# Kernel tuning notes

Measured on AMD Instinct MI355X. Metric: run time of the kernel, lower is better.

The kernel has to match this reference:

```python
import jax, jax.numpy as jnp
import numpy as np

BETA = 0.99
TOL = 1e-4
MAX_ITER = 1000
EPS = 1e-3
B, N, HF, HV, KV = 65536, 32, 25, 128, 8


def fhat(x, fp):
    W1, b1, W2, b2, W3, b3 = fp
    h = jax.nn.softplus(x @ W1 + b1)
    h = jax.nn.softplus(h @ W2 + b2)
    return h @ W3 + b3  # (B,1,N)


def V(z, vp):
    # Lyapunov function: V(z) = ||g(z)-g(0)||^2 + eps*||z||^2 ; V(0)=0, V>0 elsewhere.
    W1, b1, W2, b2, W3, b3 = vp
    def mlp(u):
        h = jax.nn.softplus(u @ W1 + b1)
        h = jax.nn.softplus(h @ W2 + b2)
        return h @ W3 + b3
    h = mlp(z)
    h0 = mlp(jnp.zeros((1, 1, z.shape[-1]), z.dtype))
    return (jnp.sum((h - h0) ** 2, axis=-1, keepdims=True)
            + EPS * jnp.sum(z * z, axis=-1, keepdims=True))  # (B,1,1)


def newton_F(fhatx, target, gamma, vp):
    # F = gamma - (V(fhatx*gamma)-target)/dV_dgamma  (newton_iter.forward)
    Vg, dV = jax.jvp(lambda g: V(fhatx * g, vp), (gamma,), (jnp.ones_like(gamma),))
    return gamma - (Vg - target) / dV


def solve_gamma(fhatx, target, vp):
    # Vectorized masked Newton + bisection (rootfind_train.forward).
    gamma = jnp.ones((fhatx.shape[0], 1, 1), fhatx.dtype)
    e1 = jnp.zeros_like(gamma)
    e2 = jnp.ones_like(gamma)
    active = (V(fhatx, vp) - target) > 0.0  # samples needing rootfind

    def cond(s):
        return jnp.logical_and(jnp.any(s[3]), s[4] < MAX_ITER)

    def body(s):
        gamma, e1, e2, m, it = s
        # Newton step on active, unconverged samples
        newt = newton_F(fhatx, target, gamma, vp)
        gamma = jnp.where(m, newt, gamma)
        # bisection backup where Newton left [e1,e2] (or produced non-finite)
        m_bisec = m & ((gamma < e1) | (gamma > e2) | ~jnp.isfinite(gamma))
        a = 0.5 * (e1 + e2)
        s_a = jnp.sign(V(fhatx * a, vp) - target)
        s_1 = jnp.sign(V(fhatx * e1, vp) - target)
        s_2 = jnp.sign(V(fhatx * e2, vp) - target)
        e2 = jnp.where(m_bisec & (s_a * s_1 < 0), a, e2)
        e1 = jnp.where(m_bisec & (s_a * s_2 < 0), a, e1)
        gamma = jnp.where(m_bisec, a, gamma)
        m = active & (jnp.abs(V(fhatx * gamma, vp) - target) > TOL)
        return (gamma, e1, e2, m, it + 1)

    gamma = jax.lax.while_loop(cond, body, (gamma, e1, e2, active, jnp.int32(0)))[0]
    return gamma


@jax.jit
def _forward(x, fp, vp):
    fhatx = fhat(x, fp)
    target = BETA * V(x, vp)
    viol = V(fhatx, vp) > target  # these go through rootfind; rest pass through fhat
    gamma = solve_gamma(fhatx, target, vp)
    return jnp.where(viol, fhatx * gamma, fhatx)


def setup_inputs() -> dict:
    key = jax.random.key(0)
    ks = jax.random.split(key, 13)
    def w(k, shape, fan):
        return jax.random.normal(k, shape, jnp.float32) / np.float32(np.sqrt(fan))
    return {
        'x': jax.random.normal(ks[0], (B, 1, N), jnp.float32),
        'f_W1': w(ks[1], (N, HF), N), 'f_b1': jnp.zeros((HF,), jnp.float32),
        'f_W2': w(ks[2], (HF, HF), HF), 'f_b2': jnp.zeros((HF,), jnp.float32),
        'f_W3': w(ks[3], (HF, N), HF), 'f_b3': jnp.zeros((N,), jnp.float32),
        'v_W1': w(ks[4], (N, HV), N), 'v_b1': jnp.zeros((HV,), jnp.float32),
        'v_W2': w(ks[5], (HV, HV), HV), 'v_b2': jnp.zeros((HV,), jnp.float32),
        'v_W3': w(ks[6], (HV, KV), HV), 'v_b3': jnp.zeros((KV,), jnp.float32),
    }


def reference(x, f_W1, f_b1, f_W2, f_b2, f_W3, f_b3,
              v_W1, v_b1, v_W2, v_b2, v_W3, v_b3):
    fp = (f_W1, f_b1, f_W2, f_b2, f_W3, f_b3)
    vp = (v_W1, v_b1, v_W2, v_b2, v_W3, v_b3)
    return _forward(x, fp, vp)
```

## Files before the change

### kernel.cpp

```cpp
#include <hip/hip_runtime.h>
#include <math.h>

#define BETA_C   0.99f
#define TOL_C    1e-4f
#define ACC_C    2e-3f
#define BRK_C    2e-3f
#define FORCE_C  6
#define MAXIT_C  1000
#define EPS_C    1e-3f
#define BN       65536
#define NN       32
#define HFD      25
#define HVD      128
#define KVD      8
#define G        16
#define GPB      16
#define SGPB     16
#define SBLK     256
#define NQBLK    768


typedef __attribute__((ext_vector_type(8))) short bf16x8;
typedef __attribute__((ext_vector_type(8))) unsigned short u16x8;
typedef __attribute__((ext_vector_type(4))) float f32x4;

__device__ __forceinline__ void wsync() {
    __builtin_amdgcn_wave_barrier();
    __threadfence_block();
    __builtin_amdgcn_wave_barrier();
}

__device__ __forceinline__ float sp_(float x) {
    return fmaxf(x, 0.f) + log1pf(expf(-fabsf(x)));
}
__device__ __forceinline__ float spf_(float x) {
    return fmaxf(x, 0.f) + __logf(1.f + __expf(-fabsf(x)));
}
__device__ __forceinline__ float sgn_(float d) {
    return (d > 0.f) ? 1.f : ((d < 0.f) ? -1.f : 0.f);
}
__device__ __forceinline__ unsigned short f2bf(float f) {
    unsigned int u = __float_as_uint(f);
    u += 0x7FFFu + ((u >> 16) & 1u);
    return (unsigned short)(u >> 16);
}
__device__ __forceinline__ float bf2f(unsigned short u) {
    return __uint_as_float(((unsigned int)u) << 16);
}

__device__ __forceinline__ void aw_st(unsigned short* aw, int row, int col, float v) {
    const int b = (row * 64 + col * 2) ^ ((row & 3) << 4);
    *(unsigned short*)((char*)aw + b) = f2bf(v);
}
__device__ __forceinline__ bf16x8 aw_ld(const unsigned short* aw, int row, int k) {
    const int b = (row * 64 + k * 2) ^ ((row & 3) << 4);
    return *(const bf16x8*)((const char*)aw + b);
}
__device__ __forceinline__ void hw_st(unsigned short* hw, int row, int col, float v) {
    const int b = (row * 256 + col * 2) ^ ((row & 7) << 4);
    *(unsigned short*)((char*)hw + b) = f2bf(v);
}
__device__ __forceinline__ bf16x8 hw_ld(const unsigned short* hw, int row, int k) {
    const int b = (row * 256 + k * 2) ^ ((row & 7) << 4);
    return *(const bf16x8*)((const char*)hw + b);
}

__device__ __forceinline__ void veval2_sec(
    const int gl, const float (&uA)[8], const float (&uB)[8],
    const float gA, const float gB,
    float2* h1q, const float n2A, const float n2B,
    const float (&b1v)[8], const float (&b2v)[8], const float (&d0c)[8],
    const unsigned short* w2L, const unsigned short* __restrict__ w3s,
    float& VA, float& VB)
{
    const int k0 = gl * 8;
#pragma unroll
    for (int j = 0; j < 8; ++j) {
        const float preA = fmaf(gA, uA[j], b1v[j]);
        const float preB = fmaf(gB, uB[j], b1v[j]);
        h1q[(j << 4) | gl] = make_float2(spf_(preA), spf_(preB));
    }
    wsync();
    float aA[8], aB[8];
#pragma unroll
    for (int j = 0; j < 8; ++j) { aA[j] = 0.f; aB[j] = 0.f; }
#pragma unroll 4
    for (int k = 0; k < HVD; ++k) {
        const float2 q = h1q[((k & 7) << 4) | (k >> 3)];
        const u16x8 wv = *(const u16x8*)(w2L + k * HVD + k0);
#pragma unroll
        for (int j = 0; j < 8; ++j) {
            const float w = bf2f(wv[j]);
            aA[j] = fmaf(q.x, w, aA[j]);
            aB[j] = fmaf(q.y, w, aB[j]);
        }
    }
    wsync();
    float oA[KVD], oB[KVD];
#pragma unroll
    for (int c = 0; c < KVD; ++c) { oA[c] = 0.f; oB[c] = 0.f; }
#pragma unroll
    for (int j = 0; j < 8; ++j) {
        const float h2A = spf_(aA[j] + b2v[j]);
        const float h2B = spf_(aB[j] + b2v[j]);
        const u16x8 w3v = *(const u16x8*)(w3s + (k0 + j) * KVD);
#pragma unroll
        for (int c = 0; c < 8; ++c) {
            const float w3 = bf2f(w3v[c]);
            oA[c] = fmaf(h2A, w3, oA[c]);
            oB[c] = fmaf(h2B, w3, oB[c]);
        }
    }
#pragma unroll
    for (int m = 1; m < G; m <<= 1) {
#pragma unroll
        for (int c = 0; c < KVD; ++c) {
            oA[c] += __shfl_xor(oA[c], m);
            oB[c] += __shfl_xor(oB[c], m);
        }
    }
    float vvA = 0.f, vvB = 0.f;
#pragma unroll
    for (int c = 0; c < KVD; ++c) {
        const float eA = oA[c] + d0c[c];
        const float eB = oB[c] + d0c[c];
        vvA = fmaf(eA, eA, vvA);
        vvB = fmaf(eB, eB, vvB);
    }
    VA = vvA + EPS_C * gA * gA * n2A;
    VB = vvB + EPS_C * gB * gB * n2B;
}

__global__ __launch_bounds__(256, 2) void k_wprep(
    const float* __restrict__ vW1, const float* __restrict__ vW2,
    const float* __restrict__ vW3,
    const float* __restrict__ vb1, const float* __restrict__ vb2,
    const float* __restrict__ vb3,
    unsigned short* __restrict__ w1b, unsigned short* __restrict__ w2b,
    unsigned short* __restrict__ w3b,
    unsigned short* __restrict__ w2s, unsigned short* __restrict__ w3s,
    float* __restrict__ h0g)
{
    if (blockIdx.x == 32) {
        __shared__ float h1s[HVD];
        __shared__ float h2p[2][HVD];
        __shared__ float h2s[HVD];
        __shared__ float o3p[16][KVD + 1];
        const int t = threadIdx.x;
        if (t < HVD) h1s[t] = sp_(vb1[t]);
        __syncthreads();
        {
            const int j = t & 127, half = t >> 7;
            float a = half ? 0.f : vb2[j];
            const int kb = half * 64;
            for (int k = 0; k < 64; ++k)
                a = fmaf(h1s[kb + k], vW2[(kb + k) * HVD + j], a);
            h2p[half][j] = a;
        }
        __syncthreads();
        if (t < HVD) h2s[t] = sp_(h2p[0][t] + h2p[1][t]);
        __syncthreads();
        if (t < 128) {
            const int c = t & 7, ch = t >> 3;
            float a = 0.f;
            for (int k = ch * 8; k < ch * 8 + 8; ++k)
                a = fmaf(h2s[k], vW3[k * KVD + c], a);
            o3p[ch][c] = a;
        }
        __syncthreads();
        if (t < KVD) {
            float acc = vb3[t];
            for (int ch = 0; ch < 16; ++ch) acc += o3p[ch][t];
            h0g[t] = acc;
        }
        return;
    }
    const int t = blockIdx.x * 256 + threadIdx.x;
    const int nth = 32 * 256;
    for (int i = t; i < HVD * NN; i += nth) {
        const int col = i >> 5, k = i & 31;
        w1b[i] = f2bf(vW1[k * HVD + col]);
    }
    for (int i = t; i < HVD * HVD; i += nth) {
        const int col = i >> 7, k = i & 127;
        w2b[i] = f2bf(vW2[k * HVD + col]);
    }
    for (int i = t; i < 16 * HVD; i += nth) {
        const int c = i >> 7, k = i & 127;
        w3b[i] = (c < KVD) ? f2bf(vW3[k * KVD + c]) : (unsigned short)0;
    }
    for (int i = t; i < HVD * HVD; i += nth)
        w2s[i] = f2bf(vW2[i]);
    for (int i = t; i < HVD * KVD; i += nth)
        w3s[i] = f2bf(vW3[i]);
}

__global__ __launch_bounds__(256, 2) void k_setup(
    const float* __restrict__ x_g,
    const float* __restrict__ fW1, const float* __restrict__ fb1,
    const float* __restrict__ fW2, const float* __restrict__ fb2,
    const float* __restrict__ fW3, const float* __restrict__ fb3,
    const float* __restrict__ vb1, const float* __restrict__ vb2,
    const float* __restrict__ vb3,
    const unsigned short* __restrict__ w1b,
    const unsigned short* __restrict__ w2b,
    const unsigned short* __restrict__ w3b,
    const float* __restrict__ h0g,
    float* __restrict__ out,
    int* __restrict__ cnt, int* __restrict__ list, float* __restrict__ tgt,
    float* __restrict__ vfb)
{
    __shared__ float2 xs[GPB][NN + 1];
    __shared__ float2 fh1[GPB][HFD + 1];
    __shared__ float2 fh2[GPB][HFD + 1];
    __shared__ __align__(16) unsigned short abf[4][16 * 32];
    __shared__ __align__(16) unsigned short hbf[4][16 * HVD];
    __shared__ int wcnt[4];
    __shared__ int bbase;

    const int tid = threadIdx.x;
    const int gi = tid >> 4;
    const int gl = tid & (G - 1);
    const int w  = tid >> 6;
    const int l  = tid & 63;
    const int q  = l >> 4;
    const int cc = l & 15;
    const int sb = (blockIdx.x * GPB + gi) * 2;
    const int s0 = sb, s1 = sb + 1;
    unsigned short* aw = abf[w];
    unsigned short* hw = hbf[w];

    const float xa0 = x_g[(size_t)s0 * NN + gl];
    const float xa1 = x_g[(size_t)s0 * NN + gl + 16];
    const float xb0 = x_g[(size_t)s1 * NN + gl];
    const float xb1 = x_g[(size_t)s1 * NN + gl + 16];
    xs[gi][gl]      = make_float2(xa0, xb0);
    xs[gi][gl + 16] = make_float2(xa1, xb1);
    const int r0 = 4 * q;
    aw_st(aw, r0,     gl,      xa0); aw_st(aw, r0,     gl + 16, xa1);
    aw_st(aw, r0 + 2, gl,      xb0); aw_st(aw, r0 + 2, gl + 16, xb1);
    wsync();

    float fA0, fA1, fB0, fB1;
    {
        const int uu0 = gl;
        const int uu1 = gl + G;
        const bool u1v = (uu1 < HFD);
        const int uu1c = u1v ? uu1 : (HFD - 1);
        float a0 = fb1[uu0], a1 = a0;
        float c0 = fb1[uu1c], c1 = c0;
#pragma unroll
        for (int i = 0; i < NN; ++i) {
            const float2 xv2 = xs[gi][i];
            const float w0 = fW1[i * HFD + uu0];
            const float w1 = fW1[i * HFD + uu1c];
            a0 = fmaf(xv2.x, w0, a0);
            a1 = fmaf(xv2.y, w0, a1);
            c0 = fmaf(xv2.x, w1, c0);
            c1 = fmaf(xv2.y, w1, c1);
        }
        fh1[gi][uu0] = make_float2(spf_(a0), spf_(a1));
        if (u1v) fh1[gi][uu1] = make_float2(spf_(c0), spf_(c1));
        wsync();
        a0 = fb2[uu0]; a1 = a0;
        c0 = fb2[uu1c]; c1 = c0;
#pragma unroll
        for (int i = 0; i < HFD; ++i) {
            const float2 h = fh1[gi][i];
            const float w0 = fW2[i * HFD + uu0];
            const float w1 = fW2[i * HFD + uu1c];
            a0 = fmaf(h.x, w0, a0);
            a1 = fmaf(h.y, w0, a1);
            c0 = fmaf(h.x, w1, c0);
            c1 = fmaf(h.y, w1, c1);
        }
        fh2[gi][uu0] = make_float2(spf_(a0), spf_(a1));
        if (u1v) fh2[gi][uu1] = make_float2(spf_(c0), spf_(c1));
        wsync();
    }
    {
        float A0 = fb3[gl], A1 = fb3[gl + 16];
        float B0 = A0,      B1 = A1;
#pragma unroll
        for (int i = 0; i < HFD; ++i) {
            const float2 h = fh2[gi][i];
            const float wa = fW3[i * NN + gl];
            const float wb = fW3[i * NN + gl + 16];
            A0 = fmaf(h.x, wa, A0); A1 = fmaf(h.x, wb, A1);
            B0 = fmaf(h.y, wa, B0); B1 = fmaf(h.y, wb, B1);
        }
        out[(size_t)s0 * NN + gl]      = A0;
        out[(size_t)s0 * NN + gl + 16] = A1;
        out[(size_t)s1 * NN + gl]      = B0;
        out[(size_t)s1 * NN + gl + 16] = B1;
        aw_st(aw, r0 + 1, gl, A0); aw_st(aw, r0 + 1, gl + 16, A1);
        aw_st(aw, r0 + 3, gl, B0); aw_st(aw, r0 + 3, gl + 16, B1);
        fA0 = A0; fA1 = A1; fB0 = B0; fB1 = B1;
    }
    wsync();

    float p0 = fmaf(xa0, xa0, xa1 * xa1);
    float p1 = fmaf(fA0, fA0, fA1 * fA1);
    float p2 = fmaf(xb0, xb0, xb1 * xb1);
    float p3 = fmaf(fB0, fB0, fB1 * fB1);
#pragma unroll
    for (int m = 1; m < G; m <<= 1) {
        p0 += __shfl_xor(p0, m); p1 += __shfl_xor(p1, m);
        p2 += __shfl_xor(p2, m); p3 += __shfl_xor(p3, m);
    }

    float b1v[8], b2v[8];
#pragma unroll
    for (int n = 0; n < 8; ++n) {
        b1v[n] = vb1[n * 16 + cc];
        b2v[n] = vb2[n * 16 + cc];
    }

    const int kq = (l >> 4) * 8;
    const f32x4 zf = {0.f, 0.f, 0.f, 0.f};

    const bf16x8 afr = aw_ld(aw, cc, kq);
    f32x4 acc1[8];
#pragma unroll
    for (int n = 0; n < 8; ++n) {
        const bf16x8 bfr = *(const bf16x8*)(w1b + (n * 16 + cc) * 32 + kq);
        acc1[n] = __builtin_amdgcn_mfma_f32_16x16x32_bf16(afr, bfr, zf, 0, 0, 0);
    }
#pragma unroll
    for (int n = 0; n < 8; ++n) {
#pragma unroll
        for (int r = 0; r < 4; ++r)
            hw_st(hw, r0 + r, n * 16 + cc, spf_(acc1[n][r] + b1v[n]));
    }
    wsync();

    f32x4 acc2[8];
#pragma unroll
    for (int n = 0; n < 8; ++n) acc2[n] = zf;
#pragma unroll
    for (int c = 0; c < 4; ++c) {
        const bf16x8 a2f = hw_ld(hw, cc, c * 32 + kq);
#pragma unroll
        for (int n = 0; n < 8; ++n) {
            const bf16x8 b2f = *(const bf16x8*)(w2b + (n * 16 + cc) * HVD + c * 32 + kq);
            acc2[n] = __builtin_amdgcn_mfma_f32_16x16x32_bf16(a2f, b2f, acc2[n], 0, 0, 0);
        }
    }
    wsync();
#pragma unroll
    for (int n = 0; n < 8; ++n) {
#pragma unroll
        for (int r = 0; r < 4; ++r)
            hw_st(hw, r0 + r, n * 16 + cc, spf_(acc2[n][r] + b2v[n]));
    }
    wsync();

    f32x4 acc3 = zf;
#pragma unroll
    for (int c = 0; c < 4; ++c) {
        const bf16x8 a3f = hw_ld(hw, cc, c * 32 + kq);
        const bf16x8 b3f = *(const bf16x8*)(w3b + cc * HVD + c * 32 + kq);
        acc3 = __builtin_amdgcn_mfma_f32_16x16x32_bf16(a3f, b3f, acc3, 0, 0, 0);
    }

    const float d0 = (cc < KVD) ? (vb3[cc] - h0g[cc]) : 0.f;
    float s_[4];
#pragma unroll
    for (int r = 0; r < 4; ++r) {
        const float e = (cc < KVD) ? (acc3[r] + d0) : 0.f;
        s_[r] = e * e;
    }
#pragma unroll
    for (int m = 1; m < G; m <<= 1) {
#pragma unroll
        for (int r = 0; r < 4; ++r) s_[r] += __shfl_xor(s_[r], m);
    }
    const float Vx0 = s_[0] + EPS_C * p0;
    const float Vf0 = s_[1] + EPS_C * p1;
    const float Vx1 = s_[2] + EPS_C * p2;
    const float Vf1 = s_[3] + EPS_C * p3;

    const float t0 = BETA_C * Vx0;
    const float t1 = BETA_C * Vx1;
    const bool act0 = (Vf0 - t0) > 0.f;
    const bool act1 = (Vf1 - t1) > 0.f;

    const bool lead = (gl == 0 && act0) || (gl == 1 && act1);
    unsigned long long bal = __ballot(lead);
    const int lane = threadIdx.x & 63, wv = threadIdx.x >> 6;
    const int rank = __popcll(bal & ((1ull << lane) - 1ull));
    if (lane == 0) wcnt[wv] = __popcll(bal);
    __syncthreads();
    if (threadIdx.x == 0) {
        int tot = 0;
        for (int i = 0; i < 4; ++i) { int c = wcnt[i]; wcnt[i] = tot; tot += c; }
        bbase = atomicAdd(cnt, tot);
    }
    __syncthreads();
    if (lead) {
        const int p = bbase + wcnt[wv] + rank;
        if (p < BN) {
            list[p] = (gl == 0) ? s0 : s1;
            tgt[p]  = (gl == 0) ? t0 : t1;
            vfb[p]  = (gl == 0) ? Vf0 : Vf1;
        }
    }
}

__global__ __launch_bounds__(SBLK, 2) void k_solve(
    const float* __restrict__ vW1, const float* __restrict__ vb1,
    const unsigned short* __restrict__ w2s, const float* __restrict__ vb2,
    const unsigned short* __restrict__ w3s, const float* __restrict__ vb3,
    const float* __restrict__ h0g,
    float* __restrict__ out,
    const int* __restrict__ cnt, const int* __restrict__ list,
    const float* __restrict__ tgt, const float* __restrict__ vfb,
    int* __restrict__ qhead)
{
    __shared__ __align__(16) unsigned short w2L[HVD * HVD];
    __shared__ __align__(8) float2 h1s[SGPB][HVD];

    {
        const uint4* s2 = (const uint4*)w2s;
        uint4* d2 = (uint4*)w2L;
        for (int i = threadIdx.x; i < (HVD * HVD) / 8; i += SBLK) d2[i] = s2[i];
    }
    __syncthreads();

    const int gi = threadIdx.x >> 4;
    const int gl = threadIdx.x & (G - 1);
    int n = *cnt;
    if (n > BN) n = BN;
    if (n < 0)  n = 0;
    float2* h1q = h1s[gi];
    const int lead = threadIdx.x & 48;

    const int k0 = gl * 8;
    float b1v[8], b2v[8], d0c[8];
    {
        const float4 a = *(const float4*)(vb1 + k0);
        const float4 b = *(const float4*)(vb1 + k0 + 4);
        b1v[0]=a.x; b1v[1]=a.y; b1v[2]=a.z; b1v[3]=a.w;
        b1v[4]=b.x; b1v[5]=b.y; b1v[6]=b.z; b1v[7]=b.w;
        const float4 c = *(const float4*)(vb2 + k0);
        const float4 d = *(const float4*)(vb2 + k0 + 4);
        b2v[0]=c.x; b2v[1]=c.y; b2v[2]=c.z; b2v[3]=c.w;
        b2v[4]=d.x; b2v[5]=d.y; b2v[6]=d.z; b2v[7]=d.w;
#pragma unroll
        for (int cix = 0; cix < KVD; ++cix) d0c[cix] = vb3[cix] - h0g[cix];
    }

    int sA, sB; float tgA, tgB, fA0, fA1, fB0, fB1, n2A, n2B;
    float uA[8], uB[8];
    float gA, e1A, e2A, vA1, vA2, pgA, pvA;
    float gB, e1B, e2B, vB1, vB2, pgB, pvB;
    bool doneA, doneB;
    int itA, itB, obhA, obhB;

    auto grab = [&]() -> bool {
        int v = 0;
        if (gl == 0) v = atomicAdd(qhead, 2);
        v = __shfl(v, lead);
        if (v >= n) return false;
        const bool hasB = (v + 1) < n;
        sA = list[v]; tgA = tgt[v];
        const float vfA = vfb[v];
        float vfB;
        if (hasB) { sB = list[v + 1]; tgB = tgt[v + 1]; vfB = vfb[v + 1]; }
        else      { sB = sA;          tgB = tgA;        vfB = vfA; }
        fA0 = out[(size_t)sA * NN + gl];
        fA1 = out[(size_t)sA * NN + gl + 16];
        fB0 = out[(size_t)sB * NN + gl];
        fB1 = out[(size_t)sB * NN + gl + 16];
        float pa = fmaf(fA0, fA0, fA1 * fA1);
        float pb = fmaf(fB0, fB0, fB1 * fB1);
#pragma unroll
        for (int m = 1; m < G; m <<= 1) {
            pa += __shfl_xor(pa, m);
            pb += __shfl_xor(pb, m);
        }
        n2A = pa; n2B = pb;
#pragma unroll
        for (int j = 0; j < 8; ++j) { uA[j] = 0.f; uB[j] = 0.f; }
#pragma unroll
        for (int i = 0; i < NN; ++i) {
            const int src = lead + (i & 15);
            const float qx = __shfl((i < 16) ? fA0 : fA1, src);
            const float qy = __shfl((i < 16) ? fB0 : fB1, src);
            const float4 wa = *(const float4*)(vW1 + i * HVD + k0);
            const float4 wb = *(const float4*)(vW1 + i * HVD + k0 + 4);
            uA[0] = fmaf(qx, wa.x, uA[0]); uA[1] = fmaf(qx, wa.y, uA[1]);
            uA[2] = fmaf(qx, wa.z, uA[2]); uA[3] = fmaf(qx, wa.w, uA[3]);
            uA[4] = fmaf(qx, wb.x, uA[4]); uA[5] = fmaf(qx, wb.y, uA[5]);
            uA[6] = fmaf(qx, wb.z, uA[6]); uA[7] = fmaf(qx, wb.w, uA[7]);
            uB[0] = fmaf(qy, wa.x, uB[0]); uB[1] = fmaf(qy, wa.y, uB[1]);
            uB[2] = fmaf(qy, wa.z, uB[2]); uB[3] = fmaf(qy, wa.w, uB[3]);
            uB[4] = fmaf(qy, wb.x, uB[4]); uB[5] = fmaf(qy, wb.y, uB[5]);
            uB[6] = fmaf(qy, wb.z, uB[6]); uB[7] = fmaf(qy, wb.w, uB[7]);
        }
        gA = sqrtf(tgA / vfA); e1A = 0.f; e2A = 1.f; vA1 = 0.f; vA2 = vfA;
        pgA = 1.f; pvA = vfA;
        gB = sqrtf(tgB / vfB); e1B = 0.f; e2B = 1.f; vB1 = 0.f; vB2 = vfB;
        pgB = 1.f; pvB = vfB;
        doneA = false; itA = 0; obhA = 0;
        doneB = !hasB; itB = 0; obhB = 0;
        return true;
    };
    if (!grab()) return;

    auto step = [&](bool& done, float& gamma, float& pg, float& pv,
                    float& e1, float& e2, float& v_e1, float& v_e2,
                    int& it, int& obh,
                    const float vp, const float target,
                    const int s, const float f0, const float f1) {
        if (done) return;
        if (fabsf(vp - target) <= TOL_C || (e2 - e1) <= BRK_C) {
            out[(size_t)s * NN + gl]      = f0 * gamma;
            out[(size_t)s * NN + gl + 16] = f1 * gamma;
            done = true;
            return;
        }
        const float sa = sgn_(vp - target);
        const float s1 = sgn_(v_e1 - target);
        if (sa * s1 < 0.f) { e2 = gamma; v_e2 = vp; }
        else               { e1 = gamma; v_e1 = vp; }
        ++it;
        const float newt = gamma - (vp - target) * (gamma - pg) / (vp - pv);
        pg = gamma; pv = vp;
        if (it < FORCE_C && newt >= e1 && newt <= e2) {
            if (fabsf(newt - gamma) <= ACC_C) {
                out[(size_t)s * NN + gl]      = f0 * newt;
                out[(size_t)s * NN + gl + 16] = f1 * newt;
                done = true;
                return;
            }
            gamma = newt;
        } else if (newt > e2 && e2 >= 1.0f) {
            if (++obh >= 2) {
                out[(size_t)s * NN + gl]      = f0;
                out[(size_t)s * NN + gl + 16] = f1;
                done = true;
                return;
            }
            gamma = 0.5f * (e1 + e2);
        } else {
            if (it & 1) {
                gamma = 0.5f * (e1 + e2);
            } else {
                const float fr0 = (target - v_e1) / (v_e2 - v_e1);
                const float fr = fminf(fmaxf(fr0, 0.1f), 0.9f);
                gamma = fmaf(fr, e2 - e1, e1);
            }
        }
        if (it >= MAXIT_C) {
            out[(size_t)s * NN + gl]      = f0 * gamma;
            out[(size_t)s * NN + gl + 16] = f1 * gamma;
            done = true;
        }
    };

    for (;;) {
        float vpA, vpB;
        veval2_sec(gl, uA, uB, gA, gB, h1q, n2A, n2B,
                   b1v, b2v, d0c, w2L, w3s, vpA, vpB);
        step(doneA, gA, pgA, pvA, e1A, e2A, vA1, vA2, itA, obhA, vpA, tgA, sA, fA0, fA1);
        step(doneB, gB, pgB, pvB, e1B, e2B, vB1, vB2, itB, obhB, vpB, tgB, sB, fB0, fB1);
        if (doneA && doneB) {
            if (!grab()) break;
        }
    }
}

extern "C" void kernel_launch(void* const* d_in, const int* in_sizes, int n_in,
                              void* d_out, int out_size, void* d_ws, size_t ws_size,
                              hipStream_t stream)
{
    const float* x   = (const float*)d_in[0];
    const float* fW1 = (const float*)d_in[1];
    const float* fb1 = (const float*)d_in[2];
    const float* fW2 = (const float*)d_in[3];
    const float* fb2 = (const float*)d_in[4];
    const float* fW3 = (const float*)d_in[5];
    const float* fb3 = (const float*)d_in[6];
    const float* vW1 = (const float*)d_in[7];
    const float* vb1 = (const float*)d_in[8];
    const float* vW2 = (const float*)d_in[9];
    const float* vb2 = (const float*)d_in[10];
    const float* vW3 = (const float*)d_in[11];
    const float* vb3 = (const float*)d_in[12];
    float* out = (float*)d_out;

    char* ws = (char*)d_ws;
    int*   cnt   = (int*)ws;
    int*   qhead = (int*)(ws + 4);
    float* h0g   = (float*)(ws + 64);
    int*   list  = (int*)(ws + 128);
    float* tgt   = (float*)(ws + 128 + (size_t)BN * 4);
    float* vfb   = (float*)(ws + 128 + (size_t)BN * 8);
    unsigned short* w1b = (unsigned short*)(ws + 128 + (size_t)BN * 12);
    unsigned short* w2b = w1b + HVD * NN;
    unsigned short* w3b = w2b + HVD * HVD;
    unsigned short* w2s = w3b + 16 * HVD;
    unsigned short* w3s = w2s + HVD * HVD;

    hipMemsetAsync(ws, 0, 8, stream);

    hipLaunchKernelGGL(k_wprep, dim3(33), dim3(256), 0, stream,
                       vW1, vW2, vW3, vb1, vb2, vb3,
                       w1b, w2b, w3b, w2s, w3s, h0g);

    hipLaunchKernelGGL(k_setup, dim3(BN / (GPB * 2)), dim3(256), 0, stream,
                       x, fW1, fb1, fW2, fb2, fW3, fb3,
                       vb1, vb2, vb3, w1b, w2b, w3b,
                       h0g, out, cnt, list, tgt, vfb);

    hipLaunchKernelGGL(k_solve, dim3(NQBLK), dim3(SBLK), 0, stream,
                       vW1, vb1, w2s, vb2, w3s, vb3,
                       h0g, out, cnt, list, tgt, vfb, qhead);
}
```

Before: 294.2 us.

## Defer slow-converging samples to a second pure-bisection solve kernel

The solve kernel now caps each sample pair at a small number of rounds. Samples still unconverged after the cap are pushed, with their current bracket, to a spill queue. A second kernel then finishes them with plain bisection using the same persistent work-queue scheme. The aim is to stop a few long-tail samples from holding a 16-lane group busy while others idle, so load balances better. The cost is an extra launch, re-loading fhat and recomputing layer-1 activations for spilled samples, and a switch to plain bisection that may change iteration counts or final values. The new path is taken only when the workspace is large enough.

```diff
diff --git a/kernel.cpp b/kernel.cpp
--- a/kernel.cpp
+++ b/kernel.cpp
@@ -6,6 +6,7 @@
 #define ACC_C    2e-3f
 #define BRK_C    2e-3f
 #define FORCE_C  6
+#define MAX1_C   6
 #define MAXIT_C  1000
 #define EPS_C    1e-3f
 #define BN       65536
@@ -415,7 +416,9 @@
     float* __restrict__ out,
     const int* __restrict__ cnt, const int* __restrict__ list,
     const float* __restrict__ tgt, const float* __restrict__ vfb,
-    int* __restrict__ qhead)
+    int* __restrict__ qhead,
+    int* __restrict__ sq_cnt, int* __restrict__ sidx, float2* __restrict__ sbr,
+    const int max1)
 {
     __shared__ __align__(16) unsigned short w2L[HVD * HVD];
     __shared__ __align__(8) float2 h1s[SGPB][HVD];
@@ -450,7 +453,7 @@
         for (int cix = 0; cix < KVD; ++cix) d0c[cix] = vb3[cix] - h0g[cix];
     }
 
-    int sA, sB; float tgA, tgB, fA0, fA1, fB0, fB1, n2A, n2B;
+    int sA, sB, vQ; float tgA, tgB, fA0, fA1, fB0, fB1, n2A, n2B;
     float uA[8], uB[8];
     float gA, e1A, e2A, vA1, vA2, pgA, pvA;
     float gB, e1B, e2B, vB1, vB2, pgB, pvB;
@@ -462,6 +465,7 @@
         if (gl == 0) v = atomicAdd(qhead, 2);
         v = __shfl(v, lead);
         if (v >= n) return false;
+        vQ = v;
         const bool hasB = (v + 1) < n;
         sA = list[v]; tgA = tgt[v];
         const float vfA = vfb[v];
@@ -559,14 +563,166 @@
         }
     };
 
+    int rounds = 0;
     for (;;) {
         float vpA, vpB;
         veval2_sec(gl, uA, uB, gA, gB, h1q, n2A, n2B,
                    b1v, b2v, d0c, w2L, w3s, vpA, vpB);
         step(doneA, gA, pgA, pvA, e1A, e2A, vA1, vA2, itA, obhA, vpA, tgA, sA, fA0, fA1);
         step(doneB, gB, pgB, pvB, e1B, e2B, vB1, vB2, itB, obhB, vpB, tgB, sB, fB0, fB1);
+        ++rounds;
         if (doneA && doneB) {
             if (!grab()) break;
+            rounds = 0;
+        } else if (rounds >= max1) {
+            if (gl == 0) {
+                if (!doneA) {
+                    const int qp = atomicAdd(sq_cnt, 1);
+                    if (qp < BN) { sidx[qp] = vQ; sbr[qp] = make_float2(e1A, e2A); }
+                }
+                if (!doneB) {
+                    const int qp = atomicAdd(sq_cnt, 1);
+                    if (qp < BN) { sidx[qp] = vQ + 1; sbr[qp] = make_float2(e1B, e2B); }
+                }
+            }
+            if (!grab()) break;
+            rounds = 0;
+        }
+    }
+}
+
+__global__ __launch_bounds__(SBLK, 2) void k_solve2(
+    const float* __restrict__ vW1, const float* __restrict__ vb1,
+    const unsigned short* __restrict__ w2s, const float* __restrict__ vb2,
+    const unsigned short* __restrict__ w3s, const float* __restrict__ vb3,
+    const float* __restrict__ h0g,
+    float* __restrict__ out,
+    const int* __restrict__ list, const float* __restrict__ tgt,
+    const int* __restrict__ sq_cnt, const int* __restrict__ sidx,
+    const float2* __restrict__ sbr,
+    int* __restrict__ q2head)
+{
+    __shared__ __align__(16) unsigned short w2L[HVD * HVD];
+    __shared__ __align__(8) float2 h1s[SGPB][HVD];
+
+    int n = *sq_cnt;
+    if (n > BN) n = BN;
+    if (n < 0)  n = 0;
+    if (n == 0) return;
+
+    {
+        const uint4* s2 = (const uint4*)w2s;
+        uint4* d2 = (uint4*)w2L;
+        for (int i = threadIdx.x; i < (HVD * HVD) / 8; i += SBLK) d2[i] = s2[i];
+    }
+    __syncthreads();
+
+    const int gi = threadIdx.x >> 4;
+    const int gl = threadIdx.x & (G - 1);
+    float2* h1q = h1s[gi];
+    const int lead = threadIdx.x & 48;
+
+    const int k0 = gl * 8;
+    float b1v[8], b2v[8], d0c[8];
+    {
+        const float4 a = *(const float4*)(vb1 + k0);
+        const float4 b = *(const float4*)(vb1 + k0 + 4);
+        b1v[0]=a.x; b1v[1]=a.y; b1v[2]=a.z; b1v[3]=a.w;
+        b1v[4]=b.x; b1v[5]=b.y; b1v[6]=b.z; b1v[7]=b.w;
+        const float4 c = *(const float4*)(vb2 + k0);
+        const float4 d = *(const float4*)(vb2 + k0 + 4);
+        b2v[0]=c.x; b2v[1]=c.y; b2v[2]=c.z; b2v[3]=c.w;
+        b2v[4]=d.x; b2v[5]=d.y; b2v[6]=d.z; b2v[7]=d.w;
+#pragma unroll
+        for (int cix = 0; cix < KVD; ++cix) d0c[cix] = vb3[cix] - h0g[cix];
+    }
+
+    int sA, sB; float tgA, tgB, fA0, fA1, fB0, fB1, n2A, n2B;
+    float uA[8], uB[8];
+    float gA, e1A, e2A;
+    float gB, e1B, e2B;
+    bool doneA, doneB;
+
+    auto grab2 = [&]() -> bool {
+        int v = 0;
+        if (gl == 0) v = atomicAdd(q2head, 2);
+        v = __shfl(v, lead);
+        if (v >= n) return false;
+        const bool hasB = (v + 1) < n;
+        const int pA = sidx[v];
+        const float2 brA = sbr[v];
+        sA = list[pA]; tgA = tgt[pA]; e1A = brA.x; e2A = brA.y;
+        if (hasB) {
+            const int pB = sidx[v + 1];
+            const float2 brB = sbr[v + 1];
+            sB = list[pB]; tgB = tgt[pB]; e1B = brB.x; e2B = brB.y;
+        } else { sB = sA; tgB = tgA; e1B = e1A; e2B = e2A; }
+        fA0 = out[(size_t)sA * NN + gl];
+        fA1 = out[(size_t)sA * NN + gl + 16];
+        fB0 = out[(size_t)sB * NN + gl];
+        fB1 = out[(size_t)sB * NN + gl + 16];
+        float pa = fmaf(fA0, fA0, fA1 * fA1);
+        float pb = fmaf(fB0, fB0, fB1 * fB1);
+#pragma unroll
+        for (int m = 1; m < G; m <<= 1) {
+            pa += __shfl_xor(pa, m);
+            pb += __shfl_xor(pb, m);
+        }
+        n2A = pa; n2B = pb;
+#pragma unroll
+        for (int j = 0; j < 8; ++j) { uA[j] = 0.f; uB[j] = 0.f; }
+#pragma unroll
+        for (int i = 0; i < NN; ++i) {
+            const int src = lead + (i & 15);
+            const float qx = __shfl((i < 16) ? fA0 : fA1, src);
+            const float qy = __shfl((i < 16) ? fB0 : fB1, src);
+            const float4 wa = *(const float4*)(vW1 + i * HVD + k0);
+            const float4 wb = *(const float4*)(vW1 + i * HVD + k0 + 4);
+            uA[0] = fmaf(qx, wa.x, uA[0]); uA[1] = fmaf(qx, wa.y, uA[1]);
+            uA[2] = fmaf(qx, wa.z, uA[2]); uA[3] = fmaf(qx, wa.w, uA[3]);
+            uA[4] = fmaf(qx, wb.x, uA[4]); uA[5] = fmaf(qx, wb.y, uA[5]);
+            uA[6] = fmaf(qx, wb.z, uA[6]); uA[7] = fmaf(qx, wb.w, uA[7]);
+            uB[0] = fmaf(qy, wa.x, uB[0]); uB[1] = fmaf(qy, wa.y, uB[1]);
+            uB[2] = fmaf(qy, wa.z, uB[2]); uB[3] = fmaf(qy, wa.w, uB[3]);
+            uB[4] = fmaf(qy, wb.x, uB[4]); uB[5] = fmaf(qy, wb.y, uB[5]);
+            uB[6] = fmaf(qy, wb.z, uB[6]); uB[7] = fmaf(qy, wb.w, uB[7]);
+        }
+        gA = 0.5f * (e1A + e2A);
+        gB = 0.5f * (e1B + e2B);
+        doneA = false; doneB = !hasB;
+        return true;
+    };
+    if (!grab2()) return;
+
+    auto bstep = [&](bool& done, float& gamma, float& e1, float& e2,
+                     const float vp, const float target,
+                     const int s, const float f0, const float f1) {
+        if (done) return;
+        if (fabsf(vp - target) <= TOL_C) {
+            out[(size_t)s * NN + gl]      = f0 * gamma;
+            out[(size_t)s * NN + gl + 16] = f1 * gamma;
+            done = true;
+            return;
+        }
+        if (vp > target) e2 = gamma; else e1 = gamma;
+        if ((e2 - e1) <= BRK_C) {
+            const float g = 0.5f * (e1 + e2);
+            out[(size_t)s * NN + gl]      = f0 * g;
+            out[(size_t)s * NN + gl + 16] = f1 * g;
+            done = true;
+            return;
+        }
+        gamma = 0.5f * (e1 + e2);
+    };
+
+    for (;;) {
+        float vpA, vpB;
+        veval2_sec(gl, uA, uB, gA, gB, h1q, n2A, n2B,
+                   b1v, b2v, d0c, w2L, w3s, vpA, vpB);
+        bstep(doneA, gA, e1A, e2A, vpA, tgA, sA, fA0, fA1);
+        bstep(doneB, gB, e1B, e2B, vpB, tgB, sB, fB0, fB1);
+        if (doneA && doneB) {
+            if (!grab2()) break;
         }
     }
 }
@@ -593,6 +749,8 @@
     char* ws = (char*)d_ws;
     int*   cnt   = (int*)ws;
     int*   qhead = (int*)(ws + 4);
+    int*   sqc   = (int*)(ws + 8);
+    int*   q2h   = (int*)(ws + 12);
     float* h0g   = (float*)(ws + 64);
     int*   list  = (int*)(ws + 128);
     float* tgt   = (float*)(ws + 128 + (size_t)BN * 4);
@@ -602,8 +760,13 @@
     unsigned short* w3b = w2b + HVD * HVD;
     unsigned short* w2s = w3b + 16 * HVD;
     unsigned short* w3s = w2s + HVD * HVD;
-
-    hipMemsetAsync(ws, 0, 8, stream);
+    char* wend = (char*)(w3s + HVD * KVD);
+    int*    sidx = (int*)wend;
+    float2* sbr  = (float2*)(wend + (size_t)BN * 4);
+    const size_t needed = (size_t)(wend - ws) + (size_t)BN * 12;
+    const bool p2ok = ws_size >= needed;
+
+    hipMemsetAsync(ws, 0, 16, stream);
 
     hipLaunchKernelGGL(k_wprep, dim3(33), dim3(256), 0, stream,
                        vW1, vW2, vW3, vb1, vb2, vb3,
@@ -616,5 +779,12 @@
 
     hipLaunchKernelGGL(k_solve, dim3(NQBLK), dim3(SBLK), 0, stream,
                        vW1, vb1, w2s, vb2, w3s, vb3,
-                       h0g, out, cnt, list, tgt, vfb, qhead);
-}
+                       h0g, out, cnt, list, tgt, vfb, qhead,
+                       sqc, sidx, sbr, p2ok ? MAX1_C : MAXIT_C);
+
+    if (p2ok) {
+        hipLaunchKernelGGL(k_solve2, dim3(NQBLK), dim3(SBLK), 0, stream,
+                           vW1, vb1, w2s, vb2, w3s, vb3,
+                           h0g, out, list, tgt, sqc, sidx, sbr, q2h);
+    }
+}
```

Measured after the change: 297.9 us. About the same (+1.2%).

## Widen solver lane groups from 16 to 32 threads per sample pair

Applied to the files above, without the earlier changes.

Each pair of rootfinding samples is now handled by 32 lanes instead of 16. Each lane owns 4 hidden units instead of 8 and one input element instead of two. This halves per-lane serial work and register use in the V evaluation, shortening the latency of each Newton iteration. In exchange the 256-thread block holds 8 groups instead of 16, the queue block count is raised to 1024 to compensate, and every reduction needs one extra shuffle stage.

```diff
diff --git a/kernel.cpp b/kernel.cpp
--- a/kernel.cpp
+++ b/kernel.cpp
@@ -15,13 +15,15 @@
 #define KVD      8
 #define G        16
 #define GPB      16
-#define SGPB     16
+#define SG       32
+#define SGPB     8
 #define SBLK     256
-#define NQBLK    768
+#define NQBLK    1024
 
 
 typedef __attribute__((ext_vector_type(8))) short bf16x8;
 typedef __attribute__((ext_vector_type(8))) unsigned short u16x8;
+typedef __attribute__((ext_vector_type(4))) unsigned short u16x4;
 typedef __attribute__((ext_vector_type(4))) float f32x4;
 
 __device__ __forceinline__ void wsync() {
@@ -66,30 +68,30 @@
 }
 
 __device__ __forceinline__ void veval2_sec(
-    const int gl, const float (&uA)[8], const float (&uB)[8],
+    const int gl, const float (&uA)[4], const float (&uB)[4],
     const float gA, const float gB,
     float2* h1q, const float n2A, const float n2B,
-    const float (&b1v)[8], const float (&b2v)[8], const float (&d0c)[8],
+    const float (&b1v)[4], const float (&b2v)[4], const float (&d0c)[8],
     const unsigned short* w2L, const unsigned short* __restrict__ w3s,
     float& VA, float& VB)
 {
-    const int k0 = gl * 8;
-#pragma unroll
-    for (int j = 0; j < 8; ++j) {
+    const int k0 = gl * 4;
+#pragma unroll
+    for (int j = 0; j < 4; ++j) {
         const float preA = fmaf(gA, uA[j], b1v[j]);
         const float preB = fmaf(gB, uB[j], b1v[j]);
-        h1q[(j << 4) | gl] = make_float2(spf_(preA), spf_(preB));
+        h1q[(j << 5) | gl] = make_float2(spf_(preA), spf_(preB));
     }
     wsync();
-    float aA[8], aB[8];
-#pragma unroll
-    for (int j = 0; j < 8; ++j) { aA[j] = 0.f; aB[j] = 0.f; }
+    float aA[4], aB[4];
+#pragma unroll
+    for (int j = 0; j < 4; ++j) { aA[j] = 0.f; aB[j] = 0.f; }
 #pragma unroll 4
     for (int k = 0; k < HVD; ++k) {
-        const float2 q = h1q[((k & 7) << 4) | (k >> 3)];
-        const u16x8 wv = *(const u16x8*)(w2L + k * HVD + k0);
-#pragma unroll
-        for (int j = 0; j < 8; ++j) {
+        const float2 q = h1q[((k & 3) << 5) | (k >> 2)];
+        const u16x4 wv = *(const u16x4*)(w2L + k * HVD + k0);
+#pragma unroll
+        for (int j = 0; j < 4; ++j) {
             const float w = bf2f(wv[j]);
             aA[j] = fmaf(q.x, w, aA[j]);
             aB[j] = fmaf(q.y, w, aB[j]);
@@ -100,7 +102,7 @@
 #pragma unroll
     for (int c = 0; c < KVD; ++c) { oA[c] = 0.f; oB[c] = 0.f; }
 #pragma unroll
-    for (int j = 0; j < 8; ++j) {
+    for (int j = 0; j < 4; ++j) {
         const float h2A = spf_(aA[j] + b2v[j]);
         const float h2B = spf_(aB[j] + b2v[j]);
         const u16x8 w3v = *(const u16x8*)(w3s + (k0 + j) * KVD);
@@ -112,7 +114,7 @@
         }
     }
 #pragma unroll
-    for (int m = 1; m < G; m <<= 1) {
+    for (int m = 1; m < SG; m <<= 1) {
 #pragma unroll
         for (int c = 0; c < KVD; ++c) {
             oA[c] += __shfl_xor(oA[c], m);
@@ -427,31 +429,27 @@
     }
     __syncthreads();
 
-    const int gi = threadIdx.x >> 4;
-    const int gl = threadIdx.x & (G - 1);
+    const int gi = threadIdx.x >> 5;
+    const int gl = threadIdx.x & (SG - 1);
     int n = *cnt;
     if (n > BN) n = BN;
     if (n < 0)  n = 0;
     float2* h1q = h1s[gi];
-    const int lead = threadIdx.x & 48;
-
-    const int k0 = gl * 8;
-    float b1v[8], b2v[8], d0c[8];
+    const int lead = threadIdx.x & 32;
+
+    const int k0 = gl * 4;
+    float b1v[4], b2v[4], d0c[8];
     {
         const float4 a = *(const float4*)(vb1 + k0);
-        const float4 b = *(const float4*)(vb1 + k0 + 4);
         b1v[0]=a.x; b1v[1]=a.y; b1v[2]=a.z; b1v[3]=a.w;
-        b1v[4]=b.x; b1v[5]=b.y; b1v[6]=b.z; b1v[7]=b.w;
         const float4 c = *(const float4*)(vb2 + k0);
-        const float4 d = *(const float4*)(vb2 + k0 + 4);
         b2v[0]=c.x; b2v[1]=c.y; b2v[2]=c.z; b2v[3]=c.w;
-        b2v[4]=d.x; b2v[5]=d.y; b2v[6]=d.z; b2v[7]=d.w;
 #pragma unroll
         for (int cix = 0; cix < KVD; ++cix) d0c[cix] = vb3[cix] - h0g[cix];
     }
 
-    int sA, sB; float tgA, tgB, fA0, fA1, fB0, fB1, n2A, n2B;
-    float uA[8], uB[8];
+    int sA, sB; float tgA, tgB, fA, fB, n2A, n2B;
+    float uA[4], uB[4];
     float gA, e1A, e2A, vA1, vA2, pgA, pvA;
     float gB, e1B, e2B, vB1, vB2, pgB, pvB;
     bool doneA, doneB;
@@ -468,35 +466,27 @@
         float vfB;
         if (hasB) { sB = list[v + 1]; tgB = tgt[v + 1]; vfB = vfb[v + 1]; }
         else      { sB = sA;          tgB = tgA;        vfB = vfA; }
-        fA0 = out[(size_t)sA * NN + gl];
-        fA1 = out[(size_t)sA * NN + gl + 16];
-        fB0 = out[(size_t)sB * NN + gl];
-        fB1 = out[(size_t)sB * NN + gl + 16];
-        float pa = fmaf(fA0, fA0, fA1 * fA1);
-        float pb = fmaf(fB0, fB0, fB1 * fB1);
-#pragma unroll
-        for (int m = 1; m < G; m <<= 1) {
+        fA = out[(size_t)sA * NN + gl];
+        fB = out[(size_t)sB * NN + gl];
+        float pa = fA * fA;
+        float pb = fB * fB;
+#pragma unroll
+        for (int m = 1; m < SG; m <<= 1) {
             pa += __shfl_xor(pa, m);
             pb += __shfl_xor(pb, m);
         }
         n2A = pa; n2B = pb;
 #pragma unroll
-        for (int j = 0; j < 8; ++j) { uA[j] = 0.f; uB[j] = 0.f; }
+        for (int j = 0; j < 4; ++j) { uA[j] = 0.f; uB[j] = 0.f; }
 #pragma unroll
         for (int i = 0; i < NN; ++i) {
-            const int src = lead + (i & 15);
-            const float qx = __shfl((i < 16) ? fA0 : fA1, src);
-            const float qy = __shfl((i < 16) ? fB0 : fB1, src);
+            const float qx = __shfl(fA, lead + i);
+            const float qy = __shfl(fB, lead + i);
             const float4 wa = *(const float4*)(vW1 + i * HVD + k0);
-            const float4 wb = *(const float4*)(vW1 + i * HVD + k0 + 4);
             uA[0] = fmaf(qx, wa.x, uA[0]); uA[1] = fmaf(qx, wa.y, uA[1]);
             uA[2] = fmaf(qx, wa.z, uA[2]); uA[3] = fmaf(qx, wa.w, uA[3]);
-            uA[4] = fmaf(qx, wb.x, uA[4]); uA[5] = fmaf(qx, wb.y, uA[5]);
-            uA[6] = fmaf(qx, wb.z, uA[6]); uA[7] = fmaf(qx, wb.w, uA[7]);
             uB[0] = fmaf(qy, wa.x, uB[0]); uB[1] = fmaf(qy, wa.y, uB[1]);
             uB[2] = fmaf(qy, wa.z, uB[2]); uB[3] = fmaf(qy, wa.w, uB[3]);
-            uB[4] = fmaf(qy, wb.x, uB[4]); uB[5] = fmaf(qy, wb.y, uB[5]);
-            uB[6] = fmaf(qy, wb.z, uB[6]); uB[7] = fmaf(qy, wb.w, uB[7]);
         }
         gA = sqrtf(tgA / vfA); e1A = 0.f; e2A = 1.f; vA1 = 0.f; vA2 = vfA;
         pgA = 1.f; pvA = vfA;
@@ -512,11 +502,10 @@
                     float& e1, float& e2, float& v_e1, float& v_e2,
                     int& it, int& obh,
                     const float vp, const float target,
-                    const int s, const float f0, const float f1) {
+                    const int s, const float f0) {
         if (done) return;
         if (fabsf(vp - target) <= TOL_C || (e2 - e1) <= BRK_C) {
-            out[(size_t)s * NN + gl]      = f0 * gamma;
-            out[(size_t)s * NN + gl + 16] = f1 * gamma;
+            out[(size_t)s * NN + gl] = f0 * gamma;
             done = true;
             return;
         }
@@ -529,16 +518,14 @@
         pg = gamma; pv = vp;
         if (it < FORCE_C && newt >= e1 && newt <= e2) {
             if (fabsf(newt - gamma) <= ACC_C) {
-                out[(size_t)s * NN + gl]      = f0 * newt;
-                out[(size_t)s * NN + gl + 16] = f1 * newt;
+                out[(size_t)s * NN + gl] = f0 * newt;
                 done = true;
                 return;
             }
             gamma = newt;
         } else if (newt > e2 && e2 >= 1.0f) {
             if (++obh >= 2) {
-                out[(size_t)s * NN + gl]      = f0;
-                out[(size_t)s * NN + gl + 16] = f1;
+                out[(size_t)s * NN + gl] = f0;
                 done = true;
                 return;
             }
@@ -553,8 +540,7 @@
             }
         }
         if (it >= MAXIT_C) {
-            out[(size_t)s * NN + gl]      = f0 * gamma;
-            out[(size_t)s * NN + gl + 16] = f1 * gamma;
+            out[(size_t)s * NN + gl] = f0 * gamma;
             done = true;
         }
     };
@@ -563,8 +549,8 @@
         float vpA, vpB;
         veval2_sec(gl, uA, uB, gA, gB, h1q, n2A, n2B,
                    b1v, b2v, d0c, w2L, w3s, vpA, vpB);
-        step(doneA, gA, pgA, pvA, e1A, e2A, vA1, vA2, itA, obhA, vpA, tgA, sA, fA0, fA1);
-        step(doneB, gB, pgB, pvB, e1B, e2B, vB1, vB2, itB, obhB, vpB, tgB, sB, fB0, fB1);
+        step(doneA, gA, pgA, pvA, e1A, e2A, vA1, vA2, itA, obhA, vpA, tgA, sA, fA);
+        step(doneB, gB, pgB, pvB, e1B, e2B, vB1, vB2, itB, obhB, vpB, tgB, sB, fB);
         if (doneA && doneB) {
             if (!grab()) break;
         }
```

New measurement: 322.2 us. 1.1x slower.
